# Kernel optimization log

Hardware: AMD Instinct MI355X
Metric: run time of the kernel (lower is better)

Reference implementation:

```python
import jax, jax.numpy as jnp
import numpy as np

EPS = 1e-5

def conv2d(x, w, b=None, pad=0):
    # x: NCHW, w: OIHW
    y = jax.lax.conv_general_dilated(x, w, (1, 1), [(pad, pad), (pad, pad)],
                                     dimension_numbers=('NCHW', 'OIHW', 'NCHW'))
    if b is not None:
        y = y + b[None, :, None, None]
    return y

def bn(x, g, beta, mean, var):
    scale = g / jnp.sqrt(var + EPS)
    return x * scale[None, :, None, None] + (beta - mean * scale)[None, :, None, None]

def conv_block(x, w, b, g, beta, mean, var):
    # two (conv3x3 + BN + ReLU) stages, params stacked on leading dim 2
    for i in range(2):
        x = jax.nn.relu(bn(conv2d(x, w[i], b[i], pad=1), g[i], beta[i], mean[i], var[i]))
    return x


def setup_inputs() -> dict:
    key = jax.random.key(0)
    ks = jax.random.split(key, 24)
    C, B, H, W = 128, 4, 56, 56
    f32 = jnp.float32
    d = {}
    d['x1'] = jax.random.normal(ks[0], (B, C, H, W), f32)
    d['x2'] = jax.random.normal(ks[1], (B, 4 * C, H, W), f32)
    d['ws'] = jax.random.normal(ks[2], (C, 4 * C, 3, 3), f32) * 0.05
    d['bs'] = jax.random.normal(ks[3], (C,), f32) * 0.05
    d['sg'] = jax.random.uniform(ks[4], (C,), f32)
    d['sbeta'] = jax.random.normal(ks[5], (C,), f32) * 0.05
    d['smean'] = jax.random.normal(ks[6], (C,), f32) * 0.05
    d['svar'] = jax.random.uniform(ks[7], (C,), f32)
    d['wq1'] = jax.random.normal(ks[8], (C, C, 1, 1), f32) * 0.05
    d['wq2'] = jax.random.normal(ks[9], (C, C, 1, 1), f32) * 0.05
    d['v1w'] = jax.random.normal(ks[10], (2, C, C, 3, 3), f32) * 0.05
    d['v1b'] = jax.random.normal(ks[11], (2, C), f32) * 0.05
    d['v1g'] = jax.random.uniform(ks[12], (2, C), f32)
    d['v1beta'] = jax.random.normal(ks[13], (2, C), f32) * 0.05
    d['v1mean'] = jax.random.normal(ks[14], (2, C), f32) * 0.05
    d['v1var'] = jax.random.uniform(ks[15], (2, C), f32)
    d['v2w'] = jax.random.normal(ks[16], (2, C, C, 3, 3), f32) * 0.05
    d['v2b'] = jax.random.normal(ks[17], (2, C), f32) * 0.05
    d['v2g'] = jax.random.uniform(ks[18], (2, C), f32)
    d['v2beta'] = jax.random.normal(ks[19], (2, C), f32) * 0.05
    d['v2mean'] = jax.random.normal(ks[20], (2, C), f32) * 0.05
    d['v2var'] = jax.random.uniform(ks[21], (2, C), f32)
    return d


def reference(x1, x2, ws, bs, sg, sbeta, smean, svar, wq1, wq2,
              v1w, v1b, v1g, v1beta, v1mean, v1var,
              v2w, v2b, v2g, v2beta, v2mean, v2var):
    x2_o = x2
    # conv_s: conv3x3 (4C->C) + BN + ReLU
    x2 = jax.nn.relu(bn(conv2d(x2, ws, bs, pad=1), sg, sbeta, smean, svar))
    B_, C, H, W = x1.shape
    N = H * W
    x1_q = conv2d(x1, wq1)              # [B,C,H,W]
    x2_q = conv2d(x2, wq2)
    x1_v = conv_block(x1, v1w, v1b, v1g, v1beta, v1mean, v1var)
    x2_v = conv_block(x2, v2w, v2b, v2g, v2beta, v2mean, v2var)
    x1_q_flat = x1_q.reshape(B_, C, N)
    x2_q_flat = x2_q.reshape(B_, C, N)
    x2_v_flat = x2_v.reshape(B_, C, N)
    # A[b,n,m] = sum_c x1_q[b,c,n] * x2_q[b,c,m]   -> [B, N1, N2]
    A = jnp.einsum('bcn,bcm->bnm', x1_q_flat, x2_q_flat)
    A = jax.nn.softmax(A, axis=1)                 # softmax over N1 (dim=1)
    # B = softmax(A^T, dim=1) == softmax over N2, then transposed -> [B, N2, N1]
    Bmat = jnp.swapaxes(jax.nn.softmax(A, axis=2), 1, 2)
    # x1_att = bmm(x2_v_flat [B,C,N2], Bmat [B,N2,N1]) -> [B,C,N1]
    x1_att = jnp.einsum('bcm,bmn->bcn', x2_v_flat, Bmat).reshape(B_, C, H, W)
    input1_att = x1_att + x1
    input2_att = x2_o
    return (input1_att, input2_att)
```

## Files before the change

kernel.cpp:

```cpp
#include <hip/hip_runtime.h>
#include <cstdint>
#include <cstddef>

using bfr8 = __attribute__((ext_vector_type(8))) short;
using sh4  = __attribute__((ext_vector_type(4))) short;
using fx4  = __attribute__((ext_vector_type(4))) float;

#define DI __device__ __forceinline__
#define MFMA16(a,b,c) __builtin_amdgcn_mfma_f32_16x16x32_bf16((a),(b),(c),0,0,0)

DI short f2bf(float f){
  unsigned u = __float_as_uint(f);
  return (short)((u + 0x7fffu + ((u >> 16) & 1u)) >> 16);
}
DI float bf2f(short s){
  return __uint_as_float(((unsigned)(unsigned short)s) << 16);
}
DI fx4 fzero(){ fx4 z; z[0]=0.f; z[1]=0.f; z[2]=0.f; z[3]=0.f; return z; }
DI bfr8 bzero(){ bfr8 z; 
  z[0]=0; z[1]=0; z[2]=0; z[3]=0; z[4]=0; z[5]=0; z[6]=0; z[7]=0; return z; }

__global__ void prep_kernel(
    const float* __restrict__ x1, const float* __restrict__ x2,
    const float* __restrict__ wsw, const float* __restrict__ bs,
    const float* __restrict__ sg, const float* __restrict__ sbeta,
    const float* __restrict__ smean, const float* __restrict__ svar,
    const float* __restrict__ wq1, const float* __restrict__ wq2,
    const float* __restrict__ v2w, const float* __restrict__ v2bias,
    const float* __restrict__ v2g, const float* __restrict__ v2beta,
    const float* __restrict__ v2mean, const float* __restrict__ v2var,
    short* __restrict__ x2bf, short* __restrict__ x1T,
    short* __restrict__ wsbf, short* __restrict__ wv2a, short* __restrict__ wv2b,
    short* __restrict__ wq1b, short* __restrict__ wq2b,
    float* __restrict__ consts, float* __restrict__ out1copy, int legacy)
{
  const int gsz = gridDim.x * blockDim.x;
  const int gid = blockIdx.x * blockDim.x + threadIdx.x;

  for (int i = gid; i < 1605632; i += gsz){
    float4 v = ((const float4*)x2)[i];
    ((float4*)out1copy)[i] = v;
    if (legacy){
      sh4 o; o[0]=f2bf(v.x); o[1]=f2bf(v.y); o[2]=f2bf(v.z); o[3]=f2bf(v.w);
      ((sh4*)x2bf)[i] = o;
    }
  }
  if (legacy){
    for (int t = gid; t < 200704; t += gsz){
      int g = t & 15; int nn = t >> 4;
      int b = nn / 3136, n = nn - b*3136;
      bfr8 o;
      #pragma unroll
      for (int k = 0; k < 8; ++k)
        o[k] = f2bf(x1[(size_t)(b*128 + g*8 + k)*3136 + n]);
      *(bfr8*)&x1T[((size_t)(b*3136) + n)*128 + g*8] = o;
    }
  }
  for (int i = gid; i < 589824; i += gsz){
    int ci = i & 511; int tap = (i >> 9) % 9; int co = i / 4608;
    wsbf[i] = f2bf(wsw[(size_t)(co*512 + ci)*9 + tap]);
  }
  for (int i = gid; i < 294912; i += gsz){
    int s = i / 147456; int r = i - s*147456;
    int ci = r & 127; int tap = (r >> 7) % 9; int co = r / 1152;
    float v = v2w[(size_t)((s*128 + co)*128 + ci)*9 + tap];
    (s ? wv2b : wv2a)[r] = f2bf(v);
  }
  for (int i = gid; i < 16384; i += gsz){
    wq1b[i] = f2bf(wq1[i]); wq2b[i] = f2bf(wq2[i]);
  }
  for (int c = gid; c < 128; c += gsz){
    float a = sg[c] * rsqrtf(svar[c] + 1e-5f);
    consts[c]       = a;
    consts[128 + c] = (bs[c] - smean[c]) * a + sbeta[c];
    float a0 = v2g[c] * rsqrtf(v2var[c] + 1e-5f);
    consts[256 + c] = a0;
    consts[384 + c] = (v2bias[c] - v2mean[c]) * a0 + v2beta[c];
    float a1 = v2g[128+c] * rsqrtf(v2var[128+c] + 1e-5f);
    consts[512 + c] = a1;
    consts[640 + c] = (v2bias[128+c] - v2mean[128+c]) * a1 + v2beta[128+c];
  }
}

template<int C>
__global__ __launch_bounds__(256, 4) void transpose_cn_kernel(
    const float* __restrict__ in, short* __restrict__ out)
{
  __shared__ float t[32][65];
  const int tid = threadIdx.x, bid = blockIdx.x;
  const int nt = bid % 49, cg = (bid / 49) % (C/32), b = bid / (49*(C/32));
  const int n0 = nt*64, c0 = cg*32;

  #pragma unroll
  for (int j = 0; j < 2; ++j){
    int u = tid + 256*j;
    int row = u >> 4, col4 = u & 15;
    float4 v = *(const float4*)&in[((size_t)(b*C) + c0 + row)*3136 + n0 + col4*4];
    t[row][col4*4+0] = v.x; t[row][col4*4+1] = v.y;
    t[row][col4*4+2] = v.z; t[row][col4*4+3] = v.w;
  }
  __syncthreads();
  {
    int n = tid >> 2, cg8 = tid & 3;
    bfr8 o;
    #pragma unroll
    for (int k = 0; k < 8; ++k) o[k] = f2bf(t[cg8*8 + k][n]);
    *(bfr8*)&out[((size_t)(b*3136) + n0 + n)*C + c0 + cg8*8] = o;
  }
}

template<int CIN, int NCIB>
__global__ __launch_bounds__(256, 2) void conv3x3_split_kernel(
    const short* __restrict__ xin,
    const short* __restrict__ wt,
    float* __restrict__ pout)
{
  __shared__ short xs[4*58*40];
  __shared__ short wsh[9*64*40];

  const int tid = threadIdx.x;
  const int w = tid >> 6, lane = tid & 63, l15 = lane & 15, blk = lane >> 4;
  const int bid = blockIdx.x;
  const int rt = bid % 28, cog = (bid / 28) & 1, b = bid / 56;
  const int r0 = rt * 2;
  const int cib0 = blockIdx.y * NCIB;
  float* pbase = pout + (size_t)blockIdx.y * 1605632;

  int pixoff[7];
  #pragma unroll
  for (int pf = 0; pf < 7; ++pf){
    int p = pf*16 + l15;
    int pr = (p >= 56) ? 1 : 0;
    int pc = p - pr*56;
    pixoff[pf] = (pr*58 + pc)*40 + 8*blk;
  }
  const int wlo = (w*16 + l15)*40 + 8*blk;

  int in_act[4], in_val[4], in_lds[4], in_go[4];
  #pragma unroll
  for (int it = 0; it < 4; ++it){
    int q = it*256 + tid;
    int cg8 = q & 3, col = (q >> 2) % 58, r = q / 232;
    int grow = r0 - 1 + r, gcol = col - 1;
    in_act[it] = (q < 928);
    in_val[it] = in_act[it] && grow >= 0 && grow < 56 && gcol >= 0 && gcol < 56;
    in_lds[it] = (r*58 + col)*40 + cg8*8;
    int gr = in_val[it] ? grow : 0, gc = in_val[it] ? gcol : 0;
    in_go[it] = (b*3136 + gr*56 + gc)*CIN + cib0*32 + cg8*8;
  }
  int wt_lds[9], wt_go[9];
  #pragma unroll
  for (int it = 0; it < 9; ++it){
    int q = it*256 + tid;
    int jj = q & 3, tap = (q >> 2) % 9, co = q / 36;
    wt_lds[it] = (tap*64 + co)*40 + jj*8;
    wt_go[it] = ((cog*64 + co)*9 + tap)*CIN + cib0*32 + jj*8;
  }

  fx4 acc[7];
  #pragma unroll
  for (int pf = 0; pf < 7; ++pf) acc[pf] = fzero();

  for (int ci = 0; ci < NCIB; ++ci){
    __syncthreads();
    #pragma unroll
    for (int it = 0; it < 4; ++it){
      if (in_act[it]){
        bfr8 v = bzero();
        if (in_val[it]) v = *(const bfr8*)&xin[in_go[it]];
        *(bfr8*)&xs[in_lds[it]] = v;
        in_go[it] += 32;
      }
    }
    #pragma unroll
    for (int it = 0; it < 9; ++it){
      *(bfr8*)&wsh[wt_lds[it]] = *(const bfr8*)&wt[wt_go[it]];
      wt_go[it] += 32;
    }
    __syncthreads();
    #pragma unroll
    for (int tap = 0; tap < 9; ++tap){
      bfr8 af = *(const bfr8*)&wsh[tap*64*40 + wlo];
      const int toff = ((tap/3)*58 + (tap%3))*40;
      #pragma unroll
      for (int pf = 0; pf < 7; ++pf){
        bfr8 bf = *(const bfr8*)&xs[pixoff[pf] + toff];
        acc[pf] = MFMA16(af, bf, acc[pf]);
      }
    }
  }
  #pragma unroll
  for (int rr = 0; rr < 4; ++rr){
    int co = cog*64 + w*16 + 4*blk + rr;
    #pragma unroll
    for (int pf = 0; pf < 7; ++pf){
      int n = r0*56 + pf*16 + l15;
      pbase[(size_t)(b*128 + co)*3136 + n] = acc[pf][rr];
    }
  }
}

template<int NS, int MODE>
__global__ __launch_bounds__(256, 4) void conv_combine_kernel(
    const float* __restrict__ p, const float* __restrict__ alpha,
    const float* __restrict__ bconst, short* __restrict__ yout)
{
  __shared__ short lt[64][66];
  const int t = threadIdx.x;
  const int bid = blockIdx.x;
  const int nt = bid % 49, cog = (bid / 49) & 1, b = bid / 98;
  const int co0 = cog*64, n0 = nt*64;
  const int coL = t >> 4, ncL = (t & 15) * 4;

  #pragma unroll
  for (int rep = 0; rep < 4; ++rep){
    int co = co0 + rep*16 + coL;
    size_t base = ((size_t)(b*128) + co)*3136 + n0 + ncL;
    float4 s = *(const float4*)&p[base];
    #pragma unroll
    for (int sp = 1; sp < NS; ++sp){
      float4 a = *(const float4*)&p[(size_t)sp*1605632 + base];
      s.x += a.x; s.y += a.y; s.z += a.z; s.w += a.w;
    }
    float al = alpha[co], bc = bconst[co];
    sh4 o;
    o[0] = f2bf(fmaxf(s.x*al + bc, 0.f));
    o[1] = f2bf(fmaxf(s.y*al + bc, 0.f));
    o[2] = f2bf(fmaxf(s.z*al + bc, 0.f));
    o[3] = f2bf(fmaxf(s.w*al + bc, 0.f));
    if (MODE == 0) *(sh4*)&yout[base] = o;
    else           *(sh4*)&lt[rep*16 + coL][ncL] = o;
  }
  if (MODE == 1){
    __syncthreads();
    #pragma unroll
    for (int rep = 0; rep < 4; ++rep){
      int nn = rep*16 + (t >> 4);
      int coc = (t & 15) * 4;
      sh4 v;
      #pragma unroll
      for (int j = 0; j < 4; ++j) v[j] = lt[coc + j][nn];
      *(sh4*)&yout[((size_t)(b*3136) + n0 + nn)*128 + co0 + coc] = v;
    }
  }
}

template<int CIN, bool TSTORE>
__global__ __launch_bounds__(256, 2) void conv3x3_kernel(
    const short* __restrict__ xin, const short* __restrict__ wt,
    const float* __restrict__ alpha, const float* __restrict__ bconst,
    short* __restrict__ yout, short* __restrict__ youtT)
{
  __shared__ short xs[4*58*40];
  __shared__ short wsh[9*64*40];

  const int tid = threadIdx.x;
  const int w = tid >> 6, lane = tid & 63, l15 = lane & 15, blk = lane >> 4;
  const int bid = blockIdx.x;
  const int rt = bid % 28, cog = (bid / 28) & 1, b = bid / 56;
  const int r0 = rt * 2;

  int pixoff[7];
  #pragma unroll
  for (int pf = 0; pf < 7; ++pf){
    int p = pf*16 + l15;
    int pr = (p >= 56) ? 1 : 0;
    int pc = p - pr*56;
    pixoff[pf] = (pr*58 + pc)*40 + 8*blk;
  }
  const int wlo = (w*16 + l15)*40 + 8*blk;

  fx4 acc[7];
  #pragma unroll
  for (int pf = 0; pf < 7; ++pf) acc[pf] = fzero();

  for (int cib = 0; cib < CIN/32; ++cib){
    __syncthreads();
    #pragma unroll
    for (int it = 0; it < 4; ++it){
      int q = it*256 + tid;
      if (q < 928){
        int col = q % 58; int cg8 = (q/58) & 3; int r = q / 232;
        int grow = r0 - 1 + r;
        int gcol = col - 1;
        bfr8 v = bzero();
        if (grow >= 0 && grow < 56 && gcol >= 0 && gcol < 56){
          #pragma unroll
          for (int k = 0; k < 8; ++k)
            v[k] = xin[(size_t)(b*CIN + cib*32 + cg8*8 + k)*3136 + grow*56 + gcol];
        }
        *(bfr8*)&xs[(r*58 + col)*40 + cg8*8] = v;
      }
    }
    #pragma unroll
    for (int it = 0; it < 9; ++it){
      int q = it*256 + tid;
      int jj = q & 3; int tap = (q >> 2) % 9; int co = q / 36;
      bfr8 wv = *(const bfr8*)&wt[(size_t)((cog*64 + co)*9 + tap)*CIN + cib*32 + jj*8];
      *(bfr8*)&wsh[(tap*64 + co)*40 + jj*8] = wv;
    }
    __syncthreads();
    #pragma unroll
    for (int tap = 0; tap < 9; ++tap){
      bfr8 af = *(const bfr8*)&wsh[tap*64*40 + wlo];
      const int toff = ((tap/3)*58 + (tap%3))*40;
      #pragma unroll
      for (int pf = 0; pf < 7; ++pf){
        bfr8 bf = *(const bfr8*)&xs[pixoff[pf] + toff];
        acc[pf] = MFMA16(af, bf, acc[pf]);
      }
    }
  }
  #pragma unroll
  for (int rr = 0; rr < 4; ++rr){
    int co = cog*64 + w*16 + 4*blk + rr;
    float al = alpha[co], bc = bconst[co];
    #pragma unroll
    for (int pf = 0; pf < 7; ++pf){
      float v = fmaxf(acc[pf][rr]*al + bc, 0.f);
      short sv = f2bf(v);
      int n = r0*56 + pf*16 + l15;
      yout[(size_t)(b*128 + co)*3136 + n] = sv;
      if (TSTORE) youtT[((size_t)(b*3136) + n)*128 + co] = sv;
    }
  }
}

__global__ __launch_bounds__(256, 4) void qproj_kernel(
    const short* __restrict__ xT, const short* __restrict__ wq,
    short* __restrict__ qt)
{
  const int tid = threadIdx.x, w = tid >> 6, lane = tid & 63;
  const int l15 = lane & 15, blk = lane >> 4;
  const int b = blockIdx.x / 196, n0 = (blockIdx.x % 196) * 16;

  fx4 acc[2];
  acc[0] = fzero(); acc[1] = fzero();

  #pragma unroll
  for (int ks = 0; ks < 4; ++ks){
    bfr8 af = *(const bfr8*)&xT[((size_t)(b*3136) + n0 + l15)*128 + ks*32 + 8*blk];
    #pragma unroll
    for (int i = 0; i < 2; ++i){
      bfr8 bf = *(const bfr8*)&wq[(size_t)((w*2 + i)*16 + l15)*128 + ks*32 + 8*blk];
      acc[i] = MFMA16(af, bf, acc[i]);
    }
  }
  #pragma unroll
  for (int i = 0; i < 2; ++i){
    #pragma unroll
    for (int rr = 0; rr < 4; ++rr){
      int n = n0 + 4*blk + rr;
      qt[((size_t)(b*3136) + n)*128 + (w*2 + i)*16 + l15] = f2bf(acc[i][rr]);
    }
  }
}

__global__ __launch_bounds__(256, 3) void lse_kernel(
    const short* __restrict__ q1t, const short* __restrict__ q2t,
    float* __restrict__ pmax, float* __restrict__ psum)
{
  const int tid = threadIdx.x, w = tid >> 6, lane = tid & 63;
  const int l15 = lane & 15, blk = lane >> 4;
  const int bid = blockIdx.x;
  const int ns = bid & 3, mt = (bid >> 2) % 49, b = bid / 196;
  const int m0 = mt*64;

  bfr8 qa[4][4];
  #pragma unroll
  for (int mf = 0; mf < 4; ++mf)
    #pragma unroll
    for (int ks = 0; ks < 4; ++ks)
      qa[mf][ks] = *(const bfr8*)&q2t[((size_t)(b*3136) + m0 + mf*16 + l15)*128 + ks*32 + 8*blk];

  float vmax[4][4], vsum[4][4];
  #pragma unroll
  for (int mf = 0; mf < 4; ++mf)
    #pragma unroll
    for (int rr = 0; rr < 4; ++rr){ vmax[mf][rr] = -1e30f; vsum[mf][rr] = 0.f; }

  bfr8 qb[4], qbn[4];
  #pragma unroll
  for (int ks = 0; ks < 4; ++ks)
    qb[ks] = *(const bfr8*)&q1t[((size_t)(b*3136) + ns*784 + w*16 + l15)*128 + ks*32 + 8*blk];

  for (int c = w; c < 49; c += 4){
    const int cn = c + 4;
    if (cn < 49){
      #pragma unroll
      for (int ks = 0; ks < 4; ++ks)
        qbn[ks] = *(const bfr8*)&q1t[((size_t)(b*3136) + ns*784 + cn*16 + l15)*128 + ks*32 + 8*blk];
    }
    fx4 acc[4];
    #pragma unroll
    for (int mf = 0; mf < 4; ++mf) acc[mf] = fzero();
    #pragma unroll
    for (int ks = 0; ks < 4; ++ks)
      #pragma unroll
      for (int mf = 0; mf < 4; ++mf)
        acc[mf] = MFMA16(qa[mf][ks], qb[ks], acc[mf]);
    #pragma unroll
    for (int mf = 0; mf < 4; ++mf)
      #pragma unroll
      for (int rr = 0; rr < 4; ++rr){
        float s = acc[mf][rr];
        float d = s - vmax[mf][rr];
        float e = __expf(-fabsf(d));
        bool up = d > 0.f;
        float mlt = up ? e : 1.f;
        float add = up ? 1.f : e;
        vsum[mf][rr] = vsum[mf][rr]*mlt + add;
        vmax[mf][rr] = fmaxf(vmax[mf][rr], s);
      }
    #pragma unroll
    for (int ks = 0; ks < 4; ++ks) qb[ks] = qbn[ks];
  }
  #pragma unroll
  for (int d = 1; d < 16; d <<= 1){
    #pragma unroll
    for (int mf = 0; mf < 4; ++mf)
      #pragma unroll
      for (int rr = 0; rr < 4; ++rr){
        float om = __shfl_xor(vmax[mf][rr], d);
        float os = __shfl_xor(vsum[mf][rr], d);
        float M = fmaxf(vmax[mf][rr], om);
        vsum[mf][rr] = vsum[mf][rr]*__expf(vmax[mf][rr]-M) + os*__expf(om-M);
        vmax[mf][rr] = M;
      }
  }
  if (l15 == 0){
    const size_t base = ((size_t)(b*16 + ns*4 + w))*3136 + m0;
    #pragma unroll
    for (int mf = 0; mf < 4; ++mf)
      #pragma unroll
      for (int rr = 0; rr < 4; ++rr){
        pmax[base + mf*16 + 4*blk + rr] = vmax[mf][rr];
        psum[base + mf*16 + 4*blk + rr] = vsum[mf][rr];
      }
  }
}

__global__ void lse_merge_kernel(
    const float* __restrict__ pmax, const float* __restrict__ psum,
    float* __restrict__ Lm)
{
  int t = blockIdx.x*256 + threadIdx.x;
  if (t >= 12544) return;
  int b = t / 3136, m = t - b*3136;
  float M = -1e30f;
  #pragma unroll
  for (int r = 0; r < 16; ++r)
    M = fmaxf(M, pmax[((size_t)(b*16 + r))*3136 + m]);
  float S = 0.f;
  #pragma unroll
  for (int r = 0; r < 16; ++r){
    size_t i = ((size_t)(b*16 + r))*3136 + m;
    S += psum[i]*__expf(pmax[i] - M);
  }
  Lm[t] = M + __logf(S);
}

__global__ __launch_bounds__(256, 4) void attn3_kernel(
    const short* __restrict__ q1t, const short* __restrict__ q2t,
    const short* __restrict__ x2v, const float* __restrict__ Lm,
    short* __restrict__ part, float* __restrict__ rpart)
{
  __shared__ short q2sh[32*128];
  __shared__ short xsh[128*32];
  __shared__ short plds[4*16*40];
  __shared__ float lmsh[448];
  const int tid = threadIdx.x, w = tid >> 6, lane = tid & 63;
  const int l15 = lane & 15, blk = lane >> 4;
  const int bid = blockIdx.x;
  const int ms = bid % 7, nt = (bid / 7) % 49, b = bid / 343;
  const int m0 = ms*448;
  const int n0w = nt*64 + w*16;

  if (tid < 112)
    ((float4*)lmsh)[tid] = ((const float4*)(Lm + b*3136 + m0))[tid];

  bfr8 qb[4];
  #pragma unroll
  for (int ks = 0; ks < 4; ++ks)
    qb[ks] = *(const bfr8*)&q1t[((size_t)(b*3136) + n0w + l15)*128 + ks*32 + 8*blk];

  bfr8 stq[2], stx[2];
  auto issue = [&](int m0c){
    #pragma unroll
    for (int j = 0; j < 2; ++j){
      int u = tid + 256*j;
      stq[j] = *(const bfr8*)&q2t[((size_t)(b*3136) + m0c + (u>>4))*128 + (u&15)*8];
      stx[j] = *(const bfr8*)&x2v[((size_t)(b*128) + (u>>2))*3136 + m0c + (u&3)*8];
    }
  };
  auto write_stage = [&](){
    #pragma unroll
    for (int j = 0; j < 2; ++j){
      int u = tid + 256*j;
      int qrow = u >> 4;
      *(bfr8*)((char*)q2sh + ((qrow*256 + (u&15)*16) ^ ((qrow&7)<<4))) = stq[j];
      int xrow = u >> 2;
      *(bfr8*)((char*)xsh + ((xrow*64 + (u&3)*16) ^ ((xrow&7)<<4))) = stx[j];
    }
  };

  fx4 pacc[8];
  #pragma unroll
  for (int cf = 0; cf < 8; ++cf) pacc[cf] = fzero();
  float rsum = 0.f;

  issue(m0);

  for (int c = 0; c < 14; ++c){
    __syncthreads();
    write_stage();
    if (c < 13) issue(m0 + (c+1)*32);
    __syncthreads();

    fx4 acc[2];
    acc[0] = fzero(); acc[1] = fzero();
    #pragma unroll
    for (int ks = 0; ks < 4; ++ks){
      #pragma unroll
      for (int mf = 0; mf < 2; ++mf){
        const int row = mf*16 + l15;
        bfr8 qv = *(const bfr8*)((const char*)q2sh +
                    ((row*256 + ks*64 + 16*blk) ^ ((row&7)<<4)));
        acc[mf] = MFMA16(qv, qb[ks], acc[mf]);
      }
    }

    #pragma unroll
    for (int mf = 0; mf < 2; ++mf){
      fx4 lv = *(const fx4*)&lmsh[c*32 + mf*16 + 4*blk];
      sh4 pk;
      #pragma unroll
      for (int rr = 0; rr < 4; ++rr){
        float a1 = __expf(acc[mf][rr] - lv[rr]);
        float p  = __expf(a1);
        rsum += p;
        pk[rr] = f2bf(p);
      }
      *(sh4*)&plds[(w*16 + l15)*40 + mf*16 + 4*blk] = pk;
    }
    bfr8 pb = *(const bfr8*)&plds[(w*16 + l15)*40 + 8*blk];
    #pragma unroll
    for (int cf = 0; cf < 8; ++cf){
      const int row = cf*16 + l15;
      bfr8 av = *(const bfr8*)((const char*)xsh +
                  ((row*64 + 16*blk) ^ ((row&7)<<4)));
      pacc[cf] = MFMA16(av, pb, pacc[cf]);
    }
  }

  rsum += __shfl_xor(rsum, 16);
  rsum += __shfl_xor(rsum, 32);
  if (lane < 16)
    rpart[((size_t)(ms*4 + b))*3136 + n0w + l15] = rsum;

  #pragma unroll
  for (int cf = 0; cf < 8; ++cf)
    #pragma unroll
    for (int rr = 0; rr < 4; ++rr){
      int cc = cf*16 + 4*blk + rr;
      part[(((size_t)(ms*4 + b))*128 + cc)*3136 + n0w + l15] = f2bf(pacc[cf][rr]);
    }
}

__global__ void rtot_kernel(const float* __restrict__ rpart,
                            float* __restrict__ rinv)
{
  int t = blockIdx.x*256 + threadIdx.x;
  if (t >= 12544) return;
  int b = t / 3136, n = t - b*3136;
  float s = 0.f;
  #pragma unroll
  for (int ms = 0; ms < 7; ++ms)
    s += rpart[((size_t)(ms*4 + b))*3136 + n];
  rinv[t] = 1.0f / s;
}

__global__ __launch_bounds__(256, 8) void attn_combine_kernel(
    const short* __restrict__ part, const float* __restrict__ rinv,
    const float* __restrict__ x1, float* __restrict__ out0)
{
  int t = blockIdx.x*256 + threadIdx.x;
  int n4 = t % 784; int rest = t / 784;
  int cc = rest & 127; int b = rest >> 7;
  float4 s = {0.f,0.f,0.f,0.f};
  #pragma unroll
  for (int ms = 0; ms < 7; ++ms){
    sh4 v = *(const sh4*)&part[((((size_t)(ms*4 + b))*128 + cc)*3136) + n4*4];
    s.x += bf2f(v[0]); s.y += bf2f(v[1]); s.z += bf2f(v[2]); s.w += bf2f(v[3]);
  }
  float4 rv = ((const float4*)rinv)[b*784 + n4];
  size_t xi = ((size_t)(b*128) + cc)*784 + n4;
  float4 xv = ((const float4*)x1)[xi];
  float4 o;
  o.x = s.x*rv.x + xv.x; o.y = s.y*rv.y + xv.y;
  o.z = s.z*rv.z + xv.z; o.w = s.w*rv.w + xv.w;
  ((float4*)out0)[xi] = o;
}

__global__ __launch_bounds__(256, 2) void colstats_kernel(
    const short* __restrict__ q1t, const short* __restrict__ q2t,
    float* __restrict__ Lm)
{
  __shared__ float smax[4][16];
  __shared__ float ssum[4][16];
  const int tid = threadIdx.x, w = tid >> 6, lane = tid & 63;
  const int l15 = lane & 15, blk = lane >> 4;
  const int b = blockIdx.x / 196, m0 = (blockIdx.x % 196) * 16;

  bfr8 bfr[4];
  #pragma unroll
  for (int ks = 0; ks < 4; ++ks)
    bfr[ks] = *(const bfr8*)&q2t[((size_t)(b*3136) + m0 + l15)*128 + ks*32 + 8*blk];

  float vmax = -1e30f, vsum = 0.f;

  for (int nc = w; nc < 196; nc += 4){
    fx4 acc = fzero();
    #pragma unroll
    for (int ks = 0; ks < 4; ++ks){
      bfr8 af = *(const bfr8*)&q1t[((size_t)(b*3136) + nc*16 + l15)*128 + ks*32 + 8*blk];
      acc = MFMA16(af, bfr[ks], acc);
    }
    float cm = fmaxf(fmaxf(acc[0], acc[1]), fmaxf(acc[2], acc[3]));
    float nm = fmaxf(vmax, cm);
    float cs = __expf(acc[0]-nm) + __expf(acc[1]-nm)
             + __expf(acc[2]-nm) + __expf(acc[3]-nm);
    vsum = vsum*__expf(vmax-nm) + cs;
    vmax = nm;
  }
  #pragma unroll
  for (int d = 16; d < 64; d <<= 1){
    float om = __shfl_xor(vmax, d);
    float os = __shfl_xor(vsum, d);
    float M = fmaxf(vmax, om);
    vsum = vsum*__expf(vmax - M) + os*__expf(om - M);
    vmax = M;
  }
  if (lane < 16){ smax[w][lane] = vmax; ssum[w][lane] = vsum; }
  __syncthreads();
  if (tid < 16){
    float M = fmaxf(fmaxf(smax[0][tid], smax[1][tid]), fmaxf(smax[2][tid], smax[3][tid]));
    float S = ssum[0][tid]*__expf(smax[0][tid]-M) + ssum[1][tid]*__expf(smax[1][tid]-M)
            + ssum[2][tid]*__expf(smax[2][tid]-M) + ssum[3][tid]*__expf(smax[3][tid]-M);
    Lm[b*3136 + m0 + tid] = M + __logf(S);
  }
}

__global__ __launch_bounds__(256, 2) void attn_kernel(
    const short* __restrict__ q1t, const short* __restrict__ q2t,
    const short* __restrict__ x2v, const float* __restrict__ Lm,
    const float* __restrict__ x1, float* __restrict__ out0)
{
  __shared__ float part[8][4][4][64];
  __shared__ short plds[4][16][72];
  __shared__ float rl[4][16];
  const int tid = threadIdx.x, w = tid >> 6, lane = tid & 63;
  const int l15 = lane & 15, blk = lane >> 4;
  const int b = blockIdx.x / 196, n0 = (blockIdx.x % 196) * 16;

  bfr8 qa[4];
  #pragma unroll
  for (int ks = 0; ks < 4; ++ks)
    qa[ks] = *(const bfr8*)&q1t[((size_t)(b*3136) + n0 + l15)*128 + ks*32 + 8*blk];

  fx4 pacc[8];
  #pragma unroll
  for (int cf = 0; cf < 8; ++cf) pacc[cf] = fzero();
  float rsum[4] = {0.f, 0.f, 0.f, 0.f};

  for (int s = w; s < 49; s += 4){
    const int m0m = s*64;
    fx4 s4[4];
    #pragma unroll
    for (int mf = 0; mf < 4; ++mf) s4[mf] = fzero();
    #pragma unroll
    for (int ks = 0; ks < 4; ++ks){
      #pragma unroll
      for (int mf = 0; mf < 4; ++mf){
        bfr8 bq = *(const bfr8*)&q2t[((size_t)(b*3136) + m0m + mf*16 + l15)*128 + ks*32 + 8*blk];
        s4[mf] = MFMA16(qa[ks], bq, s4[mf]);
      }
    }
    #pragma unroll
    for (int mf = 0; mf < 4; ++mf){
      float Lv = Lm[b*3136 + m0m + mf*16 + l15];
      #pragma unroll
      for (int rr = 0; rr < 4; ++rr){
        float a1 = __expf(s4[mf][rr] - Lv);
        float p  = __expf(a1);
        rsum[rr] += p;
        plds[w][4*blk + rr][mf*16 + l15] = f2bf(p);
      }
    }
    #pragma unroll
    for (int ks2 = 0; ks2 < 2; ++ks2){
      bfr8 pb = *(const bfr8*)&plds[w][l15][ks2*32 + 8*blk];
      #pragma unroll
      for (int cf = 0; cf < 8; ++cf){
        bfr8 av = *(const bfr8*)&x2v[((size_t)(b*128) + cf*16 + l15)*3136 + m0m + ks2*32 + 8*blk];
        pacc[cf] = MFMA16(av, pb, pacc[cf]);
      }
    }
  }
  #pragma unroll
  for (int d = 1; d < 16; d <<= 1){
    #pragma unroll
    for (int rr = 0; rr < 4; ++rr) rsum[rr] += __shfl_xor(rsum[rr], d);
  }
  if (l15 == 0){
    #pragma unroll
    for (int rr = 0; rr < 4; ++rr) rl[w][4*blk + rr] = rsum[rr];
  }
  #pragma unroll
  for (int cf = 0; cf < 8; ++cf)
    #pragma unroll
    for (int rr = 0; rr < 4; ++rr)
      part[cf][rr][w][lane] = pacc[cf][rr];
  __syncthreads();

  float rtot = rl[0][l15] + rl[1][l15] + rl[2][l15] + rl[3][l15];
  float rinv = 1.0f / rtot;
  const int n = n0 + l15;
  #pragma unroll
  for (int i = 0; i < 2; ++i){
    int cf = 2*w + i;
    #pragma unroll
    for (int rr = 0; rr < 4; ++rr){
      float v = part[cf][rr][0][lane] + part[cf][rr][1][lane]
              + part[cf][rr][2][lane] + part[cf][rr][3][lane];
      int c = cf*16 + 4*blk + rr;
      size_t idx = (size_t)(b*128 + c)*3136 + n;
      out0[idx] = v*rinv + x1[idx];
    }
  }
}

extern "C" void kernel_launch(void* const* d_in, const int* in_sizes, int n_in,
                              void* d_out, int out_size, void* d_ws, size_t ws_size,
                              hipStream_t stream)
{
  (void)in_sizes; (void)n_in; (void)out_size;
  const float* x1     = (const float*)d_in[0];
  const float* x2     = (const float*)d_in[1];
  const float* wsw    = (const float*)d_in[2];
  const float* bs     = (const float*)d_in[3];
  const float* sg     = (const float*)d_in[4];
  const float* sbeta  = (const float*)d_in[5];
  const float* smean  = (const float*)d_in[6];
  const float* svar   = (const float*)d_in[7];
  const float* wq1    = (const float*)d_in[8];
  const float* wq2    = (const float*)d_in[9];
  const float* v2w    = (const float*)d_in[16];
  const float* v2bias = (const float*)d_in[17];
  const float* v2g    = (const float*)d_in[18];
  const float* v2beta = (const float*)d_in[19];
  const float* v2mean = (const float*)d_in[20];
  const float* v2var  = (const float*)d_in[21];

  char* ws = (char*)d_ws;
  auto al = [](size_t x){ return (x + 255) & ~(size_t)255; };

  const size_t sz_nc    = al((size_t)1605632*2);
  const size_t sz_x2T   = al((size_t)6422528*2);
  const size_t sz_Lm    = al((size_t)12544*4);
  const size_t sz_lsep  = al((size_t)16*12544*4);
  const size_t sz_rp    = al((size_t)28*12544*4);
  const size_t sz_cst   = al((size_t)768*4);
  const size_t sz_part  = al((size_t)7*1605632*2);
  const size_t sz_pbuf  = al((size_t)4*1605632*4);
  const size_t sz_wsbf  = al((size_t)589824*2);
  const size_t sz_wv2   = al((size_t)147456*2);
  const size_t sz_wq    = al((size_t)16384*2);

  size_t off = 0;
  const size_t o_x2v = off;  off += sz_nc;
  const size_t o_q1t = off;  off += sz_nc;
  const size_t o_q2t = off;  off += sz_nc;
  const size_t o_x1T = off;  off += sz_nc;
  const size_t o_x2s = off;  off += sz_nc;
  const size_t o_v2t = off;  off += sz_nc;
  const size_t o_Lm  = off;  off += sz_Lm;
  const size_t o_pmx = off;  off += sz_lsep;
  const size_t o_psm = off;  off += sz_lsep;
  const size_t o_rp  = off;  off += sz_rp;
  const size_t o_ri  = off;  off += sz_Lm;
  const size_t o_cst = off;  off += sz_cst;
  const size_t o_wsb = off;  off += sz_wsbf;
  const size_t o_wva = off;  off += sz_wv2;
  const size_t o_wvb = off;  off += sz_wv2;
  const size_t o_wq1 = off;  off += sz_wq;
  const size_t o_wq2 = off;  off += sz_wq;
  const size_t o_x2T = off;  off += sz_x2T;
  const size_t o_prt = off;  off += (sz_part > sz_pbuf ? sz_part : sz_pbuf);
  const size_t fast_need = off;
  const bool fast = (ws_size >= fast_need);

  float* out0 = (float*)d_out;
  float* out1 = out0 + 1605632;

  if (fast){
    short* x2v  = (short*)(ws + o_x2v);
    short* q1t  = (short*)(ws + o_q1t);
    short* q2t  = (short*)(ws + o_q2t);
    short* x1T  = (short*)(ws + o_x1T);
    short* x2s  = (short*)(ws + o_x2s);
    short* v2t  = (short*)(ws + o_v2t);
    float* Lm   = (float*)(ws + o_Lm);
    float* pmax = (float*)(ws + o_pmx);
    float* psum = (float*)(ws + o_psm);
    float* rpart= (float*)(ws + o_rp);
    float* rinv = (float*)(ws + o_ri);
    float* consts = (float*)(ws + o_cst);
    short* wsbf = (short*)(ws + o_wsb);
    short* wv2a = (short*)(ws + o_wva);
    short* wv2b = (short*)(ws + o_wvb);
    short* wq1b = (short*)(ws + o_wq1);
    short* wq2b = (short*)(ws + o_wq2);
    short* x2T  = (short*)(ws + o_x2T);
    short* part = (short*)(ws + o_prt);
    float* pbuf = (float*)(ws + o_prt);

    prep_kernel<<<2048, 256, 0, stream>>>(x1, x2, wsw, bs, sg, sbeta, smean, svar,
        wq1, wq2, v2w, v2bias, v2g, v2beta, v2mean, v2var,
        nullptr, nullptr, wsbf, wv2a, wv2b, wq1b, wq2b, consts, out1, 0);
    transpose_cn_kernel<512><<<3136, 256, 0, stream>>>(x2, x2T);
    transpose_cn_kernel<128><<<784, 256, 0, stream>>>(x1, x1T);

    conv3x3_split_kernel<512, 4><<<dim3(224,4), 256, 0, stream>>>(x2T, wsbf, pbuf);
    conv_combine_kernel<4, 1><<<392, 256, 0, stream>>>(pbuf, consts,       consts + 128, x2s);
    qproj_kernel<<<784, 256, 0, stream>>>(x1T, wq1b, q1t);
    qproj_kernel<<<784, 256, 0, stream>>>(x2s, wq2b, q2t);
    conv3x3_split_kernel<128, 2><<<dim3(224,2), 256, 0, stream>>>(x2s, wv2a, pbuf);
    conv_combine_kernel<2, 1><<<392, 256, 0, stream>>>(pbuf, consts + 256, consts + 384, v2t);
    conv3x3_split_kernel<128, 2><<<dim3(224,2), 256, 0, stream>>>(v2t, wv2b, pbuf);
    conv_combine_kernel<2, 0><<<392, 256, 0, stream>>>(pbuf, consts + 512, consts + 640, x2v);

    lse_kernel<<<784, 256, 0, stream>>>(q1t, q2t, pmax, psum);
    lse_merge_kernel<<<49, 256, 0, stream>>>(pmax, psum, Lm);
    attn3_kernel<<<1372, 256, 0, stream>>>(q1t, q2t, x2v, Lm, part, rpart);
    rtot_kernel<<<49, 256, 0, stream>>>(rpart, rinv);
    attn_combine_kernel<<<1568, 256, 0, stream>>>(part, rinv, x1, out0);
  } else {
    size_t o = 0;
    auto bump = [&](size_t bytes)->char*{ char* p = ws + o; o += al(bytes); return p; };
    short* x2bf   = (short*)bump((size_t)6422528*2);
    short* x1T    = (short*)bump((size_t)1605632*2);
    short* wsbf   = (short*)bump((size_t)589824*2);
    short* wv2a   = (short*)bump((size_t)147456*2);
    short* wv2b   = (short*)bump((size_t)147456*2);
    short* wq1b   = (short*)bump((size_t)16384*2);
    short* wq2b   = (short*)bump((size_t)16384*2);
    float* consts = (float*)bump((size_t)768*4);
    short* x2s    = (short*)bump((size_t)1605632*2);
    short* x2sT   = (short*)bump((size_t)1605632*2);
    short* q1t    = (short*)bump((size_t)1605632*2);
    short* q2t    = (short*)bump((size_t)1605632*2);
    short* v2t    = (short*)bump((size_t)1605632*2);
    short* x2v    = (short*)bump((size_t)1605632*2);
    float* Lm     = (float*)bump((size_t)12544*4);

    prep_kernel<<<2048, 256, 0, stream>>>(x1, x2, wsw, bs, sg, sbeta, smean, svar,
        wq1, wq2, v2w, v2bias, v2g, v2beta, v2mean, v2var,
        x2bf, x1T, wsbf, wv2a, wv2b, wq1b, wq2b, consts, out1, 1);
    conv3x3_kernel<512, true ><<<224, 256, 0, stream>>>(x2bf, wsbf, consts, consts + 128, x2s, x2sT);
    qproj_kernel<<<784, 256, 0, stream>>>(x1T,  wq1b, q1t);
    qproj_kernel<<<784, 256, 0, stream>>>(x2sT, wq2b, q2t);
    conv3x3_kernel<128, false><<<224, 256, 0, stream>>>(x2s, wv2a, consts + 256, consts + 384, v2t, nullptr);
    conv3x3_kernel<128, false><<<224, 256, 0, stream>>>(v2t, wv2b, consts + 512, consts + 640, x2v, nullptr);
    colstats_kernel<<<784, 256, 0, stream>>>(q1t, q2t, Lm);
    attn_kernel<<<784, 256, 0, stream>>>(q1t, q2t, x2v, Lm, x1, out0);
  }
}
```

Before: 210.3 us.

## Materialize bf16 score matrix in lse pass and reuse it in attention

The lse kernel now writes the bf16-rounded QK scores to a large workspace buffer, and the attention kernel reads them back instead of recomputing the score GEMM, using a double-buffered x2v tile. Separately, the conv3x3 kernel loads weight fragments directly from global memory into registers instead of staging them in LDS, prefetches the next input slice, and raises occupancy to 3 blocks per SIMD. The x2 output copy is folded into the transpose kernel. This trades about 79MB of extra score write plus read for dropping the recompute GEMM.

```diff
diff --git a/kernel.cpp b/kernel.cpp
--- a/kernel.cpp
+++ b/kernel.cpp
@@ -16,8 +16,11 @@
 DI float bf2f(short s){
   return __uint_as_float(((unsigned)(unsigned short)s) << 16);
 }
+DI unsigned pk2(float lo, float hi){
+  return __builtin_amdgcn_perm(__float_as_uint(hi), __float_as_uint(lo), 0x07060302u);
+}
 DI fx4 fzero(){ fx4 z; z[0]=0.f; z[1]=0.f; z[2]=0.f; z[3]=0.f; return z; }
-DI bfr8 bzero(){ bfr8 z; 
+DI bfr8 bzero(){ bfr8 z;
   z[0]=0; z[1]=0; z[2]=0; z[3]=0; z[4]=0; z[5]=0; z[6]=0; z[7]=0; return z; }
 
 __global__ void prep_kernel(
@@ -37,15 +40,13 @@
   const int gsz = gridDim.x * blockDim.x;
   const int gid = blockIdx.x * blockDim.x + threadIdx.x;
 
-  for (int i = gid; i < 1605632; i += gsz){
-    float4 v = ((const float4*)x2)[i];
-    ((float4*)out1copy)[i] = v;
-    if (legacy){
+  if (legacy){
+    for (int i = gid; i < 1605632; i += gsz){
+      float4 v = ((const float4*)x2)[i];
+      ((float4*)out1copy)[i] = v;
       sh4 o; o[0]=f2bf(v.x); o[1]=f2bf(v.y); o[2]=f2bf(v.z); o[3]=f2bf(v.w);
       ((sh4*)x2bf)[i] = o;
     }
-  }
-  if (legacy){
     for (int t = gid; t < 200704; t += gsz){
       int g = t & 15; int nn = t >> 4;
       int b = nn / 3136, n = nn - b*3136;
@@ -82,9 +83,10 @@
   }
 }
 
-template<int C>
+template<int C, bool OC>
 __global__ __launch_bounds__(256, 4) void transpose_cn_kernel(
-    const float* __restrict__ in, short* __restrict__ out)
+    const float* __restrict__ in, short* __restrict__ out,
+    float* __restrict__ out1copy)
 {
   __shared__ float t[32][65];
   const int tid = threadIdx.x, bid = blockIdx.x;
@@ -95,7 +97,9 @@
   for (int j = 0; j < 2; ++j){
     int u = tid + 256*j;
     int row = u >> 4, col4 = u & 15;
-    float4 v = *(const float4*)&in[((size_t)(b*C) + c0 + row)*3136 + n0 + col4*4];
+    size_t gi = ((size_t)(b*C) + c0 + row)*3136 + n0 + col4*4;
+    float4 v = *(const float4*)&in[gi];
+    if (OC) *(float4*)&out1copy[gi] = v;
     t[row][col4*4+0] = v.x; t[row][col4*4+1] = v.y;
     t[row][col4*4+2] = v.z; t[row][col4*4+3] = v.w;
   }
@@ -110,13 +114,12 @@
 }
 
 template<int CIN, int NCIB>
-__global__ __launch_bounds__(256, 2) void conv3x3_split_kernel(
+__global__ __launch_bounds__(256, 3) void conv3x3_split_kernel(
     const short* __restrict__ xin,
     const short* __restrict__ wt,
     float* __restrict__ pout)
 {
   __shared__ short xs[4*58*40];
-  __shared__ short wsh[9*64*40];
 
   const int tid = threadIdx.x;
   const int w = tid >> 6, lane = tid & 63, l15 = lane & 15, blk = lane >> 4;
@@ -134,7 +137,6 @@
     int pc = p - pr*56;
     pixoff[pf] = (pr*58 + pc)*40 + 8*blk;
   }
-  const int wlo = (w*16 + l15)*40 + 8*blk;
 
   int in_act[4], in_val[4], in_lds[4], in_go[4];
   #pragma unroll
@@ -148,44 +150,45 @@
     int gr = in_val[it] ? grow : 0, gc = in_val[it] ? gcol : 0;
     in_go[it] = (b*3136 + gr*56 + gc)*CIN + cib0*32 + cg8*8;
   }
-  int wt_lds[9], wt_go[9];
-  #pragma unroll
-  for (int it = 0; it < 9; ++it){
-    int q = it*256 + tid;
-    int jj = q & 3, tap = (q >> 2) % 9, co = q / 36;
-    wt_lds[it] = (tap*64 + co)*40 + jj*8;
-    wt_go[it] = ((cog*64 + co)*9 + tap)*CIN + cib0*32 + jj*8;
-  }
+  int wb = (cog*64 + w*16 + l15)*9*CIN + cib0*32 + 8*blk;
 
   fx4 acc[7];
   #pragma unroll
   for (int pf = 0; pf < 7; ++pf) acc[pf] = fzero();
+
+  bfr8 sv[4];
+  #pragma unroll
+  for (int it = 0; it < 4; ++it) sv[it] = bzero();
+  #pragma unroll
+  for (int it = 0; it < 4; ++it){
+    if (in_val[it]){ sv[it] = *(const bfr8*)&xin[in_go[it]]; in_go[it] += 32; }
+  }
 
   for (int ci = 0; ci < NCIB; ++ci){
     __syncthreads();
     #pragma unroll
     for (int it = 0; it < 4; ++it){
-      if (in_act[it]){
-        bfr8 v = bzero();
-        if (in_val[it]) v = *(const bfr8*)&xin[in_go[it]];
-        *(bfr8*)&xs[in_lds[it]] = v;
-        in_go[it] += 32;
-      }
-    }
-    #pragma unroll
-    for (int it = 0; it < 9; ++it){
-      *(bfr8*)&wsh[wt_lds[it]] = *(const bfr8*)&wt[wt_go[it]];
-      wt_go[it] += 32;
-    }
+      if (in_act[it]) *(bfr8*)&xs[in_lds[it]] = sv[it];
+    }
+    if (ci + 1 < NCIB){
+      #pragma unroll
+      for (int it = 0; it < 4; ++it){
+        if (in_val[it]){ sv[it] = *(const bfr8*)&xin[in_go[it]]; in_go[it] += 32; }
+      }
+    }
+    bfr8 af[9];
+    #pragma unroll
+    for (int tap = 0; tap < 9; ++tap)
+      af[tap] = *(const bfr8*)&wt[wb + tap*CIN];
+    wb += 32;
     __syncthreads();
     #pragma unroll
     for (int tap = 0; tap < 9; ++tap){
-      bfr8 af = *(const bfr8*)&wsh[tap*64*40 + wlo];
       const int toff = ((tap/3)*58 + (tap%3))*40;
       #pragma unroll
       for (int pf = 0; pf < 7; ++pf){
         bfr8 bf = *(const bfr8*)&xs[pixoff[pf] + toff];
-        acc[pf] = MFMA16(af, bf, acc[pf]);
+        acc[pf] = MFMA16(af[tap], bf, acc[pf]);
       }
     }
   }
@@ -358,6 +361,7 @@
 
 __global__ __launch_bounds__(256, 3) void lse_kernel(
     const short* __restrict__ q1t, const short* __restrict__ q2t,
+    short* __restrict__ Sbuf,
     float* __restrict__ pmax, float* __restrict__ psum)
 {
   const int tid = threadIdx.x, w = tid >> 6, lane = tid & 63;
@@ -399,11 +403,16 @@
       #pragma unroll
       for (int mf = 0; mf < 4; ++mf)
         acc[mf] = MFMA16(qa[mf][ks], qb[ks], acc[mf]);
-    #pragma unroll
-    for (int mf = 0; mf < 4; ++mf)
+    const size_t srow = ((size_t)(b*3136) + ns*784 + c*16 + l15)*3136 + m0;
+    #pragma unroll
+    for (int mf = 0; mf < 4; ++mf){
+      sh4 rv;
+      #pragma unroll
+      for (int rr = 0; rr < 4; ++rr) rv[rr] = f2bf(acc[mf][rr]);
+      *(sh4*)&Sbuf[srow + mf*16 + 4*blk] = rv;
       #pragma unroll
       for (int rr = 0; rr < 4; ++rr){
-        float s = acc[mf][rr];
+        float s = bf2f(rv[rr]);
         float d = s - vmax[mf][rr];
         float e = __expf(-fabsf(d));
         bool up = d > 0.f;
@@ -412,6 +421,7 @@
         vsum[mf][rr] = vsum[mf][rr]*mlt + add;
         vmax[mf][rr] = fmaxf(vmax[mf][rr], s);
       }
+    }
     #pragma unroll
     for (int ks = 0; ks < 4; ++ks) qb[ks] = qbn[ks];
   }
@@ -460,14 +470,13 @@
   Lm[t] = M + __logf(S);
 }
 
-__global__ __launch_bounds__(256, 4) void attn3_kernel(
-    const short* __restrict__ q1t, const short* __restrict__ q2t,
-    const short* __restrict__ x2v, const float* __restrict__ Lm,
+__global__ __launch_bounds__(256, 4) void attn4_kernel(
+    const short* __restrict__ S, const short* __restrict__ x2v,
+    const float* __restrict__ Lm,
     short* __restrict__ part, float* __restrict__ rpart)
 {
-  __shared__ short q2sh[32*128];
-  __shared__ short xsh[128*32];
-  __shared__ short plds[4*16*40];
+  __shared__ short xshA[128*32];
+  __shared__ short xshB[128*32];
   __shared__ float lmsh[448];
   const int tid = threadIdx.x, w = tid >> 6, lane = tid & 63;
   const int l15 = lane & 15, blk = lane >> 4;
@@ -475,82 +484,76 @@
   const int ms = bid % 7, nt = (bid / 7) % 49, b = bid / 343;
   const int m0 = ms*448;
   const int n0w = nt*64 + w*16;
+  const size_t srow = ((size_t)(b*3136) + n0w + l15)*3136 + m0 + 8*blk;
 
   if (tid < 112)
     ((float4*)lmsh)[tid] = ((const float4*)(Lm + b*3136 + m0))[tid];
 
-  bfr8 qb[4];
-  #pragma unroll
-  for (int ks = 0; ks < 4; ++ks)
-    qb[ks] = *(const bfr8*)&q1t[((size_t)(b*3136) + n0w + l15)*128 + ks*32 + 8*blk];
-
-  bfr8 stq[2], stx[2];
-  auto issue = [&](int m0c){
-    #pragma unroll
-    for (int j = 0; j < 2; ++j){
-      int u = tid + 256*j;
-      stq[j] = *(const bfr8*)&q2t[((size_t)(b*3136) + m0c + (u>>4))*128 + (u&15)*8];
-      stx[j] = *(const bfr8*)&x2v[((size_t)(b*128) + (u>>2))*3136 + m0c + (u&3)*8];
-    }
-  };
-  auto write_stage = [&](){
-    #pragma unroll
-    for (int j = 0; j < 2; ++j){
-      int u = tid + 256*j;
-      int qrow = u >> 4;
-      *(bfr8*)((char*)q2sh + ((qrow*256 + (u&15)*16) ^ ((qrow&7)<<4))) = stq[j];
-      int xrow = u >> 2;
-      *(bfr8*)((char*)xsh + ((xrow*64 + (u&3)*16) ^ ((xrow&7)<<4))) = stx[j];
-    }
-  };
+  bfr8 stx[2];
+  int sg[2], sl[2];
+  #pragma unroll
+  for (int j = 0; j < 2; ++j){
+    int u = tid + 256*j;
+    int row = u >> 2, mc = (u & 3)*16;
+    sg[j] = (b*128 + row)*3136 + m0 + (u & 3)*8;
+    sl[j] = (row*64 + mc) ^ ((row&7)<<4);
+  }
 
   fx4 pacc[8];
   #pragma unroll
   for (int cf = 0; cf < 8; ++cf) pacc[cf] = fzero();
   float rsum = 0.f;
 
-  issue(m0);
+  bfr8 svc = *(const bfr8*)&S[srow];
+  bfr8 svn = *(const bfr8*)&S[srow + 32];
+  #pragma unroll
+  for (int j = 0; j < 2; ++j) stx[j] = *(const bfr8*)&x2v[sg[j]];
+  #pragma unroll
+  for (int j = 0; j < 2; ++j) *(bfr8*)((char*)xshA + sl[j]) = stx[j];
+  #pragma unroll
+  for (int j = 0; j < 2; ++j) stx[j] = *(const bfr8*)&x2v[sg[j] + 32];
+  __syncthreads();
 
   for (int c = 0; c < 14; ++c){
-    __syncthreads();
-    write_stage();
-    if (c < 13) issue(m0 + (c+1)*32);
-    __syncthreads();
-
-    fx4 acc[2];
-    acc[0] = fzero(); acc[1] = fzero();
-    #pragma unroll
-    for (int ks = 0; ks < 4; ++ks){
-      #pragma unroll
-      for (int mf = 0; mf < 2; ++mf){
-        const int row = mf*16 + l15;
-        bfr8 qv = *(const bfr8*)((const char*)q2sh +
-                    ((row*256 + ks*64 + 16*blk) ^ ((row&7)<<4)));
-        acc[mf] = MFMA16(qv, qb[ks], acc[mf]);
-      }
-    }
-
-    #pragma unroll
-    for (int mf = 0; mf < 2; ++mf){
-      fx4 lv = *(const fx4*)&lmsh[c*32 + mf*16 + 4*blk];
-      sh4 pk;
-      #pragma unroll
-      for (int rr = 0; rr < 4; ++rr){
-        float a1 = __expf(acc[mf][rr] - lv[rr]);
-        float p  = __expf(a1);
-        rsum += p;
-        pk[rr] = f2bf(p);
-      }
-      *(sh4*)&plds[(w*16 + l15)*40 + mf*16 + 4*blk] = pk;
-    }
-    bfr8 pb = *(const bfr8*)&plds[(w*16 + l15)*40 + 8*blk];
+    short* xcur = (c & 1) ? xshB : xshA;
+    short* xnxt = (c & 1) ? xshA : xshB;
+
+    fx4 l0 = *(const fx4*)&lmsh[c*32 + 8*blk];
+    fx4 l1 = *(const fx4*)&lmsh[c*32 + 8*blk + 4];
+    float p0 = __expf(__expf(bf2f(svc[0]) - l0[0]));
+    float p1 = __expf(__expf(bf2f(svc[1]) - l0[1]));
+    float p2 = __expf(__expf(bf2f(svc[2]) - l0[2]));
+    float p3 = __expf(__expf(bf2f(svc[3]) - l0[3]));
+    float p4 = __expf(__expf(bf2f(svc[4]) - l1[0]));
+    float p5 = __expf(__expf(bf2f(svc[5]) - l1[1]));
+    float p6 = __expf(__expf(bf2f(svc[6]) - l1[2]));
+    float p7 = __expf(__expf(bf2f(svc[7]) - l1[3]));
+    rsum += ((p0+p1)+(p2+p3)) + ((p4+p5)+(p6+p7));
+    int4 pi;
+    pi.x = (int)pk2(p0, p1); pi.y = (int)pk2(p2, p3);
+    pi.z = (int)pk2(p4, p5); pi.w = (int)pk2(p6, p7);
+    bfr8 pb = *(bfr8*)&pi;
+
     #pragma unroll
     for (int cf = 0; cf < 8; ++cf){
       const int row = cf*16 + l15;
-      bfr8 av = *(const bfr8*)((const char*)xsh +
+      bfr8 av = *(const bfr8*)((const char*)xcur +
                   ((row*64 + 16*blk) ^ ((row&7)<<4)));
       pacc[cf] = MFMA16(av, pb, pacc[cf]);
     }
+
+    if (c < 13){
+      #pragma unroll
+      for (int j = 0; j < 2; ++j) *(bfr8*)((char*)xnxt + sl[j]) = stx[j];
+      svc = svn;
+      if (c < 12){
+        svn = *(const bfr8*)&S[srow + (size_t)(c+2)*32];
+        #pragma unroll
+        for (int j = 0; j < 2; ++j)
+          stx[j] = *(const bfr8*)&x2v[sg[j] + (c+2)*32];
+      }
+    }
+    __syncthreads();
   }
 
   rsum += __shfl_xor(rsum, 16);
@@ -767,6 +770,7 @@
 
   const size_t sz_nc    = al((size_t)1605632*2);
   const size_t sz_x2T   = al((size_t)6422528*2);
+  const size_t sz_S     = al((size_t)4*3136*3136*2);
   const size_t sz_Lm    = al((size_t)12544*4);
   const size_t sz_lsep  = al((size_t)16*12544*4);
   const size_t sz_rp    = al((size_t)28*12544*4);
@@ -795,8 +799,8 @@
   const size_t o_wvb = off;  off += sz_wv2;
   const size_t o_wq1 = off;  off += sz_wq;
   const size_t o_wq2 = off;  off += sz_wq;
-  const size_t o_x2T = off;  off += sz_x2T;
   const size_t o_prt = off;  off += (sz_part > sz_pbuf ? sz_part : sz_pbuf);
+  const size_t o_big = off;  off += (sz_x2T > sz_S ? sz_x2T : sz_S);
   const size_t fast_need = off;
   const bool fast = (ws_size >= fast_need);
 
@@ -821,15 +825,16 @@
     short* wv2b = (short*)(ws + o_wvb);
     short* wq1b = (short*)(ws + o_wq1);
     short* wq2b = (short*)(ws + o_wq2);
-    short* x2T  = (short*)(ws + o_x2T);
     short* part = (short*)(ws + o_prt);
     float* pbuf = (float*)(ws + o_prt);
+    short* x2T  = (short*)(ws + o_big);
+    short* Sbuf = (short*)(ws + o_big);
 
     prep_kernel<<<2048, 256, 0, stream>>>(x1, x2, wsw, bs, sg, sbeta, smean, svar,
         wq1, wq2, v2w, v2bias, v2g, v2beta, v2mean, v2var,
         nullptr, nullptr, wsbf, wv2a, wv2b, wq1b, wq2b, consts, out1, 0);
-    transpose_cn_kernel<512><<<3136, 256, 0, stream>>>(x2, x2T);
-    transpose_cn_kernel<128><<<784, 256, 0, stream>>>(x1, x1T);
+    transpose_cn_kernel<512, true ><<<3136, 256, 0, stream>>>(x2, x2T, out1);
+    transpose_cn_kernel<128, false><<<784, 256, 0, stream>>>(x1, x1T, nullptr);
 
     conv3x3_split_kernel<512, 4><<<dim3(224,4), 256, 0, stream>>>(x2T, wsbf, pbuf);
     conv_combine_kernel<4, 1><<<392, 256, 0, stream>>>(pbuf, consts,       consts + 128, x2s);
@@ -840,9 +845,9 @@
     conv3x3_split_kernel<128, 2><<<dim3(224,2), 256, 0, stream>>>(v2t, wv2b, pbuf);
     conv_combine_kernel<2, 0><<<392, 256, 0, stream>>>(pbuf, consts + 512, consts + 640, x2v);
 
-    lse_kernel<<<784, 256, 0, stream>>>(q1t, q2t, pmax, psum);
+    lse_kernel<<<784, 256, 0, stream>>>(q1t, q2t, Sbuf, pmax, psum);
     lse_merge_kernel<<<49, 256, 0, stream>>>(pmax, psum, Lm);
-    attn3_kernel<<<1372, 256, 0, stream>>>(q1t, q2t, x2v, Lm, part, rpart);
+    attn4_kernel<<<1372, 256, 0, stream>>>(Sbuf, x2v, Lm, part, rpart);
     rtot_kernel<<<49, 256, 0, stream>>>(rpart, rinv);
     attn_combine_kernel<<<1568, 256, 0, stream>>>(part, rinv, x1, out0);
   } else {
```

After: 200.2 us. -4.8%, faster.
